# Kernel tuning notes

Measured on AMD Instinct MI355X. Metric: run time of the kernel, lower is better.

The kernel has to match this reference:

```python
import jax, jax.numpy as jnp
import numpy as np

N_HEADS = 16
MAX_SEQ_LEN = 2048


def _rotary_tables(d_k, max_seq_len):
    # Rotary.__init__: dim//4 frequencies followed by dim//4 zeros -> dim//2 entries
    freqs = (1.0 / 10000.0) ** jnp.linspace(0.0, 1.0, d_k // 4, dtype=jnp.float32)
    freqs = jnp.concatenate([freqs, jnp.zeros(d_k // 4, dtype=jnp.float32)])
    theta = jnp.arange(max_seq_len, dtype=jnp.float32)[:, None] * freqs[None, :]  # [S, d_k//2]
    return jnp.cos(theta), jnp.sin(theta)


def _apply_rotary_bug_faithful(u, cos, sin):
    # u: [B, H, T, Dk]. Original Rotary indexes cos/sin by u.size(-3) == n_heads,
    # so the rotation angle depends on the HEAD index and broadcasts over time.
    H = u.shape[1]
    c = cos[None, :H, None, :]  # [1, H, 1, Dk//2]
    s = sin[None, :H, None, :]
    u1, u2 = jnp.split(u.astype(jnp.float32), 2, axis=-1)
    y1 = u1 * c + u2 * s
    y2 = -u1 * s + u2 * c
    return jnp.concatenate([y1, y2], axis=-1).astype(u.dtype)


def setup_inputs() -> dict:
    key = jax.random.key(0)
    k1, k2, k3 = jax.random.split(key, 3)
    d_model = 2048
    B, T = 2, 2048
    x = jax.random.normal(k1, (B, T, d_model), dtype=jnp.float32)
    w_qkv = jax.random.normal(k2, (3 * d_model, d_model), dtype=jnp.float32) * (1.0 / np.sqrt(d_model))
    w_o = jax.random.normal(k3, (d_model, d_model), dtype=jnp.float32) * (1.0 / np.sqrt(d_model))
    return {"x": x, "w_qkv": w_qkv, "w_o": w_o}


def reference(x, w_qkv, w_o):
    B, T, D = x.shape
    H = N_HEADS
    dk = D // H
    cos, sin = _rotary_tables(dk, MAX_SEQ_LEN)

    # Fused QKV projection (Linear, no bias): [B,T,3D]
    qkv = jnp.einsum('btd,ed->bte', x, w_qkv)
    qkv = qkv.reshape(B, T, 3, H, dk).transpose(2, 0, 3, 1, 4)  # [3,B,H,T,dk]
    Q, K, V = qkv[0], qkv[1], qkv[2]

    Q = _apply_rotary_bug_faithful(Q, cos, sin)
    K = _apply_rotary_bug_faithful(K, cos, sin)

    # Causal scaled dot-product attention (eval mode -> dropout_p = 0)
    scale = 1.0 / np.sqrt(dk)
    scores = jnp.einsum('bhqd,bhkd->bhqk', Q, K) * scale
    causal = jnp.tril(jnp.ones((T, T), dtype=bool))
    scores = jnp.where(causal[None, None], scores, jnp.finfo(scores.dtype).min)
    attn = jax.nn.softmax(scores, axis=-1)
    out = jnp.einsum('bhqk,bhkd->bhqd', attn, V)  # [B,H,T,dk]
    out = out.transpose(0, 2, 1, 3).reshape(B, T, D)
    return jnp.einsum('btd,ed->bte', out, w_o)
```

## Files before the change

kernel.cpp:

```cpp
#include <hip/hip_runtime.h>

typedef unsigned short u16;
typedef short bf16x8 __attribute__((ext_vector_type(8)));
typedef float f32x4 __attribute__((ext_vector_type(4)));
typedef unsigned short u16x4 __attribute__((ext_vector_type(4)));

#define QK_SCALE 0.08838834764831845f

__device__ __forceinline__ u16 f2bf(float f) {
  unsigned u = __float_as_uint(f);
  u += 0x7fffu + ((u >> 16) & 1u);
  return (u16)(u >> 16);
}
__device__ __forceinline__ float bf2f(u16 h) { return __uint_as_float(((unsigned)h) << 16); }

__device__ __forceinline__ void gld_lds16(const u16* g, u16* l) {
  __builtin_amdgcn_global_load_lds(
      (const __attribute__((address_space(1))) void*)g,
      (__attribute__((address_space(3))) void*)l, 16, 0, 0);
}

__global__ void cvt_bf16_kernel(const float* __restrict__ in, u16* __restrict__ out, int n4) {
  int i = blockIdx.x * 256 + threadIdx.x;
  if (i >= n4) return;
  const float4 v = reinterpret_cast<const float4*>(in)[i];
  u16x4 o;
  o[0] = f2bf(v.x); o[1] = f2bf(v.y); o[2] = f2bf(v.z); o[3] = f2bf(v.w);
  reinterpret_cast<u16x4*>(out)[i] = o;
}

template<int MODE>
__global__ __launch_bounds__(256) void gemm_bt_kernel(
    const u16* __restrict__ A, const u16* __restrict__ Bw, int Kdim, int n_out,
    u16* __restrict__ q_out, u16* __restrict__ k_out, u16* __restrict__ v_out,
    float* __restrict__ f_out)
{
  __shared__ __align__(16) u16 As[128 * 32];
  __shared__ __align__(16) u16 Bs[128 * 32];
  const int t = threadIdx.x;
  const int lane = t & 63;
  const int w = t >> 6;
  const int wr = w >> 1, wc = w & 1;
  const int m0 = blockIdx.x * 128, n0 = blockIdx.y * 128;

  f32x4 acc[4][4];
#pragma unroll
  for (int m = 0; m < 4; ++m)
#pragma unroll
    for (int n = 0; n < 4; ++n)
#pragma unroll
      for (int i = 0; i < 4; ++i) acc[m][n][i] = 0.0f;

  const int ob0 = w * 1024 + lane * 16;
  const int row0 = ob0 >> 6;
  const int cole0 = (ob0 & 63) >> 1;
  const u16* gA0 = A + (size_t)(m0 + row0) * Kdim + cole0;
  const u16* gA1 = gA0 + (size_t)64 * Kdim;
  const u16* gB0 = Bw + (size_t)(n0 + row0) * Kdim + cole0;
  const u16* gB1 = gB0 + (size_t)64 * Kdim;
  u16* lA = As + w * 512;
  u16* lB = Bs + w * 512;

  const int l15 = lane & 15;
  const int kb = (lane >> 4) * 8;

  for (int k0 = 0; k0 < Kdim; k0 += 32) {
    __syncthreads();
    gld_lds16(gA0, lA);
    gld_lds16(gA1, lA + 2048);
    gld_lds16(gB0, lB);
    gld_lds16(gB1, lB + 2048);
    gA0 += 32; gA1 += 32; gB0 += 32; gB1 += 32;
    __syncthreads();
    bf16x8 a[4], b[4];
#pragma unroll
    for (int m = 0; m < 4; ++m)
      a[m] = *reinterpret_cast<const bf16x8*>(As + (wr * 64 + m * 16 + l15) * 32 + kb);
#pragma unroll
    for (int n = 0; n < 4; ++n)
      b[n] = *reinterpret_cast<const bf16x8*>(Bs + (wc * 64 + n * 16 + l15) * 32 + kb);
#pragma unroll
    for (int m = 0; m < 4; ++m)
#pragma unroll
      for (int n = 0; n < 4; ++n)
        acc[m][n] = __builtin_amdgcn_mfma_f32_16x16x32_bf16(a[m], b[n], acc[m][n], 0, 0, 0);
  }

  const int rb = wr * 64 + ((lane >> 4) << 2);
  const int cbs = wc * 64 + l15;
  if (MODE == 0) {
#pragma unroll
    for (int n = 0; n < 4; ++n) {
      const int e = n0 + cbs + n * 16;
      const int which = e >> 11;
      const int h = (e >> 7) & 15;
      const int d = e & 127;
      u16* dst = (which == 0) ? q_out : (which == 1) ? k_out : v_out;
#pragma unroll
      for (int m = 0; m < 4; ++m)
#pragma unroll
        for (int r = 0; r < 4; ++r) {
          const int bt = m0 + rb + m * 16 + r;
          const int bb = bt >> 11, tt = bt & 2047;
          dst[((size_t)(bb * 16 + h) * 2048 + tt) * 128 + d] = f2bf(acc[m][n][r]);
        }
    }
  } else {
#pragma unroll
    for (int m = 0; m < 4; ++m)
#pragma unroll
      for (int r = 0; r < 4; ++r) {
        const int row = m0 + rb + m * 16 + r;
#pragma unroll
        for (int n = 0; n < 4; ++n)
          f_out[(size_t)row * n_out + n0 + cbs + n * 16] = acc[m][n][r];
      }
  }
}

__global__ void rotary_kernel(u16* __restrict__ Qb, u16* __restrict__ Kb) {
  const int idx = blockIdx.x * 256 + threadIdx.x;
  const int j4 = idx & 15;
  const int row = idx >> 4;
  const int h = (row >> 11) & 15;
  const size_t base = (size_t)row * 128 + j4 * 4;
  float c[4], s[4];
#pragma unroll
  for (int i = 0; i < 4; ++i) {
    const int j = j4 * 4 + i;
    const float fr = (j < 32) ? __expf(-0.2971077539f * (float)j) : 0.0f;
    const float th = (float)h * fr;
    c[i] = cosf(th); s[i] = sinf(th);
  }
  {
    u16x4 u1 = *reinterpret_cast<u16x4*>(Qb + base);
    u16x4 u2 = *reinterpret_cast<u16x4*>(Qb + base + 64);
    u16x4 y1, y2;
#pragma unroll
    for (int i = 0; i < 4; ++i) {
      const float a = bf2f(u1[i]), b = bf2f(u2[i]);
      y1[i] = f2bf((a * c[i] + b * s[i]) * QK_SCALE);
      y2[i] = f2bf((b * c[i] - a * s[i]) * QK_SCALE);
    }
    *reinterpret_cast<u16x4*>(Qb + base) = y1;
    *reinterpret_cast<u16x4*>(Qb + base + 64) = y2;
  }
  {
    u16x4 u1 = *reinterpret_cast<u16x4*>(Kb + base);
    u16x4 u2 = *reinterpret_cast<u16x4*>(Kb + base + 64);
    u16x4 y1, y2;
#pragma unroll
    for (int i = 0; i < 4; ++i) {
      const float a = bf2f(u1[i]), b = bf2f(u2[i]);
      y1[i] = f2bf(a * c[i] + b * s[i]);
      y2[i] = f2bf(b * c[i] - a * s[i]);
    }
    *reinterpret_cast<u16x4*>(Kb + base) = y1;
    *reinterpret_cast<u16x4*>(Kb + base + 64) = y2;
  }
}

__global__ void transpose_v_kernel(const u16* __restrict__ V, u16* __restrict__ Vt) {
  __shared__ u16 tile[64][65];
  const int d0 = blockIdx.x * 64;
  const int t0 = blockIdx.y * 64;
  const int bh = blockIdx.z;
  const u16* src = V + (size_t)bh * (2048 * 128);
  u16* dst = Vt + (size_t)bh * (128 * 2048);
  const int tid = threadIdx.x;
  const int c4 = (tid & 15) * 4;
  const int r0 = tid >> 4;
#pragma unroll
  for (int p = 0; p < 4; ++p) {
    const int row = r0 + p * 16;
    const u16x4 v = *reinterpret_cast<const u16x4*>(src + (size_t)(t0 + row) * 128 + d0 + c4);
    tile[row][c4] = v[0]; tile[row][c4 + 1] = v[1];
    tile[row][c4 + 2] = v[2]; tile[row][c4 + 3] = v[3];
  }
  __syncthreads();
#pragma unroll
  for (int p = 0; p < 4; ++p) {
    const int dr = r0 + p * 16;
    u16x4 ov;
    ov[0] = tile[c4][dr]; ov[1] = tile[c4 + 1][dr];
    ov[2] = tile[c4 + 2][dr]; ov[3] = tile[c4 + 3][dr];
    *reinterpret_cast<u16x4*>(dst + (size_t)(d0 + dr) * 2048 + t0 + c4) = ov;
  }
}

__global__ __launch_bounds__(256) void attn_kernel(
    const u16* __restrict__ Q, const u16* __restrict__ K,
    const u16* __restrict__ Vt, u16* __restrict__ O)
{
  __shared__ __align__(16) u16 k_lds[2][64 * 128];
  __shared__ __align__(16) u16 v_lds[2][128 * 64];
  __shared__ __align__(16) u16 p_lds[4][1024];
  const int t = threadIdx.x, lane = t & 63, w = t >> 6;
  const int bh = blockIdx.y;
  const int bx = blockIdx.x;
  const int l15 = lane & 15, lhi = lane >> 4;
  const size_t qkb = (size_t)bh * (2048 * 128);
  const u16* Kg = K + qkb;
  const u16* Vg = Vt + (size_t)bh * (size_t)(128 * 2048);
  char* pw = (char*)(&p_lds[w][0]);
  const int bb = bh >> 4, h = bh & 15;
  const int kxor = (l15 & 7) << 4;

  auto stage = [&](int buf, int k0) {
#pragma unroll
    for (int ii = 0; ii < 4; ++ii) {
      const int i = w * 4 + ii;
      const int krow = i * 4 + lhi;
      gld_lds16(Kg + (size_t)(k0 + krow) * 128 + (size_t)((l15 ^ (krow & 7)) * 8),
                &k_lds[buf][i * 512]);
    }
#pragma unroll
    for (int ii = 0; ii < 4; ++ii) {
      const int i = w * 4 + ii;
      const int vrow = i * 8 + (lane >> 3);
      gld_lds16(Vg + (size_t)vrow * 2048 + k0 + (size_t)(((lane & 7) ^ (vrow & 7)) * 8),
                &v_lds[buf][i * 512]);
    }
  };

  for (int half = 0; half < 2; ++half) {
    const int qt = half ? (31 - bx) : bx;
    const int q0 = qt * 64 + w * 16;
    bf16x8 aq[4];
    {
      const u16* qp = Q + qkb + (size_t)(q0 + l15) * 128 + lhi * 8;
#pragma unroll
      for (int ks = 0; ks < 4; ++ks) aq[ks] = *reinterpret_cast<const bf16x8*>(qp + ks * 32);
    }
    f32x4 o[8];
#pragma unroll
    for (int dt = 0; dt < 8; ++dt)
#pragma unroll
      for (int i = 0; i < 4; ++i) o[dt][i] = 0.0f;
    float mrow[4] = {-1e30f, -1e30f, -1e30f, -1e30f};
    float lrow[4] = {0.f, 0.f, 0.f, 0.f};
    const int rbase = q0 + (lhi << 2);
    const int ktmax = qt;

    __syncthreads();
    stage(0, 0);
    int cur = 0;
    for (int kt = 0; kt <= ktmax; ++kt) {
      __syncthreads();
      if (kt < ktmax) stage(cur ^ 1, (kt + 1) * 64);

      const char* kbb = (const char*)(&k_lds[cur][0]);
      f32x4 s4[4];
#pragma unroll
      for (int nt = 0; nt < 4; ++nt)
#pragma unroll
        for (int i = 0; i < 4; ++i) s4[nt][i] = 0.0f;
#pragma unroll
      for (int nt = 0; nt < 4; ++nt) {
        const int krow = nt * 16 + l15;
#pragma unroll
        for (int ks = 0; ks < 4; ++ks) {
          const bf16x8 bk = *reinterpret_cast<const bf16x8*>(
              kbb + krow * 256 + ((ks * 64 + lhi * 16) ^ kxor));
          s4[nt] = __builtin_amdgcn_mfma_f32_16x16x32_bf16(aq[ks], bk, s4[nt], 0, 0, 0);
        }
      }
      if (kt == ktmax) {
#pragma unroll
        for (int nt = 0; nt < 4; ++nt) {
          const int col = kt * 64 + nt * 16 + l15;
#pragma unroll
          for (int r = 0; r < 4; ++r)
            if (col > rbase + r) s4[nt][r] = -1e30f;
        }
      }
      float alpha[4];
#pragma unroll
      for (int r = 0; r < 4; ++r) {
        float mx = fmaxf(fmaxf(s4[0][r], s4[1][r]), fmaxf(s4[2][r], s4[3][r]));
        mx = fmaxf(mx, __shfl_xor(mx, 1));
        mx = fmaxf(mx, __shfl_xor(mx, 2));
        mx = fmaxf(mx, __shfl_xor(mx, 4));
        mx = fmaxf(mx, __shfl_xor(mx, 8));
        const float mn = fmaxf(mrow[r], mx);
        alpha[r] = __expf(mrow[r] - mn);
        mrow[r] = mn;
      }
      float ps[4] = {0.f, 0.f, 0.f, 0.f};
#pragma unroll
      for (int nt = 0; nt < 4; ++nt)
#pragma unroll
        for (int r = 0; r < 4; ++r) {
          const float p = __expf(s4[nt][r] - mrow[r]);
          ps[r] += p;
          const int prow = (lhi << 2) + r;
          const int cbyte = (nt * 16 + l15) * 2;
          *(u16*)(pw + prow * 128 + (cbyte ^ ((prow & 7) << 4))) = f2bf(p);
        }
#pragma unroll
      for (int r = 0; r < 4; ++r) {
        float rs = ps[r];
        rs += __shfl_xor(rs, 1);
        rs += __shfl_xor(rs, 2);
        rs += __shfl_xor(rs, 4);
        rs += __shfl_xor(rs, 8);
        lrow[r] = lrow[r] * alpha[r] + rs;
#pragma unroll
        for (int dt = 0; dt < 8; ++dt) o[dt][r] *= alpha[r];
      }
      const char* vbb = (const char*)(&v_lds[cur][0]);
#pragma unroll
      for (int ks2 = 0; ks2 < 2; ++ks2) {
        const bf16x8 ap = *reinterpret_cast<const bf16x8*>(
            pw + l15 * 128 + ((ks2 * 64 + (lhi << 4)) ^ kxor));
#pragma unroll
        for (int dt = 0; dt < 8; ++dt) {
          const int vrow = dt * 16 + l15;
          const bf16x8 bv = *reinterpret_cast<const bf16x8*>(
              vbb + vrow * 128 + ((ks2 * 64 + lhi * 16) ^ kxor));
          o[dt] = __builtin_amdgcn_mfma_f32_16x16x32_bf16(ap, bv, o[dt], 0, 0, 0);
        }
      }
      cur ^= 1;
    }
#pragma unroll
    for (int r = 0; r < 4; ++r) {
      const float inv = 1.0f / lrow[r];
      const int row = rbase + r;
      u16* op = O + (size_t)(bb * 2048 + row) * 2048 + h * 128 + l15;
#pragma unroll
      for (int dt = 0; dt < 8; ++dt) op[dt * 16] = f2bf(o[dt][r] * inv);
    }
  }
}

extern "C" void kernel_launch(void* const* d_in, const int* in_sizes, int n_in,
                              void* d_out, int out_size, void* d_ws, size_t ws_size,
                              hipStream_t stream) {
  const float* x = (const float*)d_in[0];
  const float* wqkv = (const float*)d_in[1];
  const float* wo = (const float*)d_in[2];
  float* out = (float*)d_out;
  u16* ws = (u16*)d_ws;

  u16* xb = ws;
  u16* wqkvb = xb + 8388608;
  u16* wob = wqkvb + 12582912;
  u16* Qb = wob + 4194304;
  u16* Kb = Qb + 8388608;
  u16* Vb = Kb + 8388608;
  u16* Vtb = wqkvb;
  u16* attn = xb;

  cvt_bf16_kernel<<<8192, 256, 0, stream>>>(x, xb, 2097152);
  cvt_bf16_kernel<<<12288, 256, 0, stream>>>(wqkv, wqkvb, 3145728);
  cvt_bf16_kernel<<<4096, 256, 0, stream>>>(wo, wob, 1048576);

  gemm_bt_kernel<0><<<dim3(32, 48), 256, 0, stream>>>(xb, wqkvb, 2048, 0, Qb, Kb, Vb, nullptr);

  rotary_kernel<<<4096, 256, 0, stream>>>(Qb, Kb);
  transpose_v_kernel<<<dim3(2, 32, 32), 256, 0, stream>>>(Vb, Vtb);

  attn_kernel<<<dim3(16, 32), 256, 0, stream>>>(Qb, Kb, Vtb, attn);

  gemm_bt_kernel<1><<<dim3(32, 16), 256, 0, stream>>>(attn, wob, 2048, 2048, nullptr, nullptr, nullptr, out);
}
```

Measured before the change: 327.2 us.

## Add 256x256 double-buffered 8-wave GEMM for the QKV projection

Replaces the QKV projection GEMM with a new kernel. It uses 256x256 output tiles, 512 threads (8 waves), K tiles of 64, double-buffered LDS with an XOR-swizzled layout, and async global-to-LDS loads that overlap the MFMA work in phases. The loop raises wave priority around the MFMA phases with s_setprio and uses explicit barriers and vmcnt waits. The goal is more data reuse per tile and hiding global load latency, in exchange for 128KB of LDS per block and more register pressure. The output projection keeps the old simple GEMM, now without the unused mode template.

After: 323.3 us. About the same (-1.2%).

```diff
diff --git a/kernel.cpp b/kernel.cpp
--- a/kernel.cpp
+++ b/kernel.cpp
@@ -30,13 +30,167 @@
 }
 
 template<int MODE>
-__global__ __launch_bounds__(256) void gemm_bt_kernel(
+__global__ __launch_bounds__(512, 2) void gemm8p_kernel(
     const u16* __restrict__ A, const u16* __restrict__ Bw, int Kdim, int n_out,
     u16* __restrict__ q_out, u16* __restrict__ k_out, u16* __restrict__ v_out,
     float* __restrict__ f_out)
 {
-  __shared__ __align__(16) u16 As[128 * 32];
-  __shared__ __align__(16) u16 Bs[128 * 32];
+  __shared__ __align__(16) u16 As[2][256 * 64];
+  __shared__ __align__(16) u16 Bs[2][256 * 64];
+  const int t = threadIdx.x, lane = t & 63, w = t >> 6;
+  const int wr = w >> 2, wc = w & 3;
+  const int l15 = lane & 15, lhi = lane >> 4;
+  const int m0 = blockIdx.x * 256, n0 = blockIdx.y * 256;
+  const int NT = Kdim >> 6;
+
+  const int srow = w * 8 + (lane >> 3);
+  const int gchunk = (lane & 7) ^ (srow & 7);
+  const size_t gcol = (size_t)gchunk * 8;
+
+  auto stageA2 = [&](int buf, int kt2, int half) {
+    const size_t kb = (size_t)kt2 * 64 + gcol;
+#pragma unroll
+    for (int i = 0; i < 2; ++i) {
+      const int ro = half * 128 + i * 64;
+      gld_lds16(A + (size_t)(m0 + srow + ro) * Kdim + kb, &As[buf][(w * 8 + ro) * 64]);
+    }
+  };
+  auto stageB4 = [&](int buf, int kt2) {
+    const size_t kb = (size_t)kt2 * 64 + gcol;
+#pragma unroll
+    for (int ro = 0; ro < 256; ro += 64)
+      gld_lds16(Bw + (size_t)(n0 + srow + ro) * Kdim + kb, &Bs[buf][(w * 8 + ro) * 64]);
+  };
+
+  const int arow0 = (wr * 128 + l15) * 64;
+  const int brow0 = (wc * 64 + l15) * 64;
+  const int koff0 = ((0 + lhi) ^ (l15 & 7)) * 8;
+  const int koff1 = ((4 + lhi) ^ (l15 & 7)) * 8;
+
+  f32x4 acc[8][4];
+#pragma unroll
+  for (int m = 0; m < 8; ++m)
+#pragma unroll
+    for (int n = 0; n < 4; ++n)
+#pragma unroll
+      for (int i = 0; i < 4; ++i) acc[m][n][i] = 0.0f;
+
+  stageA2(0, 0, 0); stageA2(0, 0, 1);
+  stageB4(0, 0);
+  if (NT > 1) { stageA2(1, 1, 0); stageA2(1, 1, 1); }
+  asm volatile("s_waitcnt vmcnt(4)" ::: "memory");
+  __builtin_amdgcn_s_barrier();
+
+  for (int kt = 0; kt < NT; ++kt) {
+    const int cur = kt & 1;
+    const u16* __restrict__ Ac = &As[cur][0];
+    const u16* __restrict__ Bc = &Bs[cur][0];
+    bf16x8 aK1[4], a2K1[4], b0[4], b1[4];
+    {
+      bf16x8 aK0[4];
+#pragma unroll
+      for (int m = 0; m < 4; ++m) {
+        aK0[m] = *reinterpret_cast<const bf16x8*>(Ac + arow0 + m * 1024 + koff0);
+        aK1[m] = *reinterpret_cast<const bf16x8*>(Ac + arow0 + m * 1024 + koff1);
+      }
+#pragma unroll
+      for (int n = 0; n < 4; ++n)
+        b0[n] = *reinterpret_cast<const bf16x8*>(Bc + brow0 + n * 1024 + koff0);
+      if (kt + 1 < NT) stageB4(cur ^ 1, kt + 1);
+      __builtin_amdgcn_s_barrier();
+      asm volatile("s_waitcnt lgkmcnt(0)" ::: "memory");
+      __builtin_amdgcn_s_setprio(1);
+#pragma unroll
+      for (int m = 0; m < 4; ++m)
+#pragma unroll
+        for (int n = 0; n < 4; ++n)
+          acc[m][n] = __builtin_amdgcn_mfma_f32_16x16x32_bf16(aK0[m], b0[n], acc[m][n], 0, 0, 0);
+      __builtin_amdgcn_s_setprio(0);
+      __builtin_amdgcn_s_barrier();
+    }
+    {
+      bf16x8 a2K0[4];
+#pragma unroll
+      for (int m = 0; m < 4; ++m) {
+        a2K0[m] = *reinterpret_cast<const bf16x8*>(Ac + arow0 + (m + 4) * 1024 + koff0);
+        a2K1[m] = *reinterpret_cast<const bf16x8*>(Ac + arow0 + (m + 4) * 1024 + koff1);
+      }
+#pragma unroll
+      for (int n = 0; n < 4; ++n)
+        b1[n] = *reinterpret_cast<const bf16x8*>(Bc + brow0 + n * 1024 + koff1);
+      __builtin_amdgcn_s_barrier();
+      asm volatile("s_waitcnt lgkmcnt(0)" ::: "memory");
+      __builtin_amdgcn_s_setprio(1);
+#pragma unroll
+      for (int m = 0; m < 4; ++m)
+#pragma unroll
+        for (int n = 0; n < 4; ++n)
+          acc[m + 4][n] = __builtin_amdgcn_mfma_f32_16x16x32_bf16(a2K0[m], b0[n], acc[m + 4][n], 0, 0, 0);
+      __builtin_amdgcn_s_setprio(0);
+      __builtin_amdgcn_s_barrier();
+    }
+    if (kt + 2 < NT) stageA2(cur, kt + 2, 0);
+    __builtin_amdgcn_s_barrier();
+    __builtin_amdgcn_s_setprio(1);
+#pragma unroll
+    for (int m = 0; m < 4; ++m)
+#pragma unroll
+      for (int n = 0; n < 4; ++n)
+        acc[m][n] = __builtin_amdgcn_mfma_f32_16x16x32_bf16(aK1[m], b1[n], acc[m][n], 0, 0, 0);
+    __builtin_amdgcn_s_setprio(0);
+    __builtin_amdgcn_s_barrier();
+    if (kt + 2 < NT) stageA2(cur, kt + 2, 1);
+    __builtin_amdgcn_s_barrier();
+    __builtin_amdgcn_s_setprio(1);
+#pragma unroll
+    for (int m = 0; m < 4; ++m)
+#pragma unroll
+      for (int n = 0; n < 4; ++n)
+        acc[m + 4][n] = __builtin_amdgcn_mfma_f32_16x16x32_bf16(a2K1[m], b1[n], acc[m + 4][n], 0, 0, 0);
+    __builtin_amdgcn_s_setprio(0);
+    if (kt < NT - 2) { asm volatile("s_waitcnt vmcnt(4)" ::: "memory"); }
+    else             { asm volatile("s_waitcnt vmcnt(0)" ::: "memory"); }
+    __builtin_amdgcn_s_barrier();
+  }
+
+  const int rb = wr * 128 + lhi * 4;
+  const int cb = wc * 64 + l15;
+  if (MODE == 0) {
+#pragma unroll
+    for (int n = 0; n < 4; ++n) {
+      const int e = n0 + cb + n * 16;
+      const int which = e >> 11;
+      const int h = (e >> 7) & 15;
+      const int d = e & 127;
+      u16* dst = (which == 0) ? q_out : (which == 1) ? k_out : v_out;
+#pragma unroll
+      for (int m = 0; m < 8; ++m)
+#pragma unroll
+        for (int r = 0; r < 4; ++r) {
+          const int bt = m0 + rb + m * 16 + r;
+          const int bb = bt >> 11, tt = bt & 2047;
+          dst[((size_t)(bb * 16 + h) * 2048 + tt) * 128 + d] = f2bf(acc[m][n][r]);
+        }
+    }
+  } else {
+#pragma unroll
+    for (int m = 0; m < 8; ++m)
+#pragma unroll
+      for (int r = 0; r < 4; ++r) {
+        const int row = m0 + rb + m * 16 + r;
+#pragma unroll
+        for (int n = 0; n < 4; ++n)
+          f_out[(size_t)row * n_out + n0 + cb + n * 16] = acc[m][n][r];
+      }
+  }
+}
+
+__global__ __launch_bounds__(256) void gemm_bt_kernel(
+    const u16* __restrict__ A, const u16* __restrict__ Bw, int Kdim, int n_out,
+    float* __restrict__ f_out)
+{
+  __shared__ __align__(16) u16 Asl[128 * 32];
+  __shared__ __align__(16) u16 Bsl[128 * 32];
   const int t = threadIdx.x;
   const int lane = t & 63;
   const int w = t >> 6;
@@ -58,8 +212,8 @@
   const u16* gA1 = gA0 + (size_t)64 * Kdim;
   const u16* gB0 = Bw + (size_t)(n0 + row0) * Kdim + cole0;
   const u16* gB1 = gB0 + (size_t)64 * Kdim;
-  u16* lA = As + w * 512;
-  u16* lB = Bs + w * 512;
+  u16* lA = Asl + w * 512;
+  u16* lB = Bsl + w * 512;
 
   const int l15 = lane & 15;
   const int kb = (lane >> 4) * 8;
@@ -75,10 +229,10 @@
     bf16x8 a[4], b[4];
 #pragma unroll
     for (int m = 0; m < 4; ++m)
-      a[m] = *reinterpret_cast<const bf16x8*>(As + (wr * 64 + m * 16 + l15) * 32 + kb);
+      a[m] = *reinterpret_cast<const bf16x8*>(Asl + (wr * 64 + m * 16 + l15) * 32 + kb);
 #pragma unroll
     for (int n = 0; n < 4; ++n)
-      b[n] = *reinterpret_cast<const bf16x8*>(Bs + (wc * 64 + n * 16 + l15) * 32 + kb);
+      b[n] = *reinterpret_cast<const bf16x8*>(Bsl + (wc * 64 + n * 16 + l15) * 32 + kb);
 #pragma unroll
     for (int m = 0; m < 4; ++m)
 #pragma unroll
@@ -88,34 +242,15 @@
 
   const int rb = wr * 64 + ((lane >> 4) << 2);
   const int cbs = wc * 64 + l15;
-  if (MODE == 0) {
-#pragma unroll
-    for (int n = 0; n < 4; ++n) {
-      const int e = n0 + cbs + n * 16;
-      const int which = e >> 11;
-      const int h = (e >> 7) & 15;
-      const int d = e & 127;
-      u16* dst = (which == 0) ? q_out : (which == 1) ? k_out : v_out;
-#pragma unroll
-      for (int m = 0; m < 4; ++m)
-#pragma unroll
-        for (int r = 0; r < 4; ++r) {
-          const int bt = m0 + rb + m * 16 + r;
-          const int bb = bt >> 11, tt = bt & 2047;
-          dst[((size_t)(bb * 16 + h) * 2048 + tt) * 128 + d] = f2bf(acc[m][n][r]);
-        }
-    }
-  } else {
-#pragma unroll
-    for (int m = 0; m < 4; ++m)
-#pragma unroll
-      for (int r = 0; r < 4; ++r) {
-        const int row = m0 + rb + m * 16 + r;
-#pragma unroll
-        for (int n = 0; n < 4; ++n)
-          f_out[(size_t)row * n_out + n0 + cbs + n * 16] = acc[m][n][r];
-      }
-  }
+#pragma unroll
+  for (int m = 0; m < 4; ++m)
+#pragma unroll
+    for (int r = 0; r < 4; ++r) {
+      const int row = m0 + rb + m * 16 + r;
+#pragma unroll
+      for (int n = 0; n < 4; ++n)
+        f_out[(size_t)row * n_out + n0 + cbs + n * 16] = acc[m][n][r];
+    }
 }
 
 __global__ void rotary_kernel(u16* __restrict__ Qb, u16* __restrict__ Kb) {
@@ -356,12 +491,12 @@
   cvt_bf16_kernel<<<12288, 256, 0, stream>>>(wqkv, wqkvb, 3145728);
   cvt_bf16_kernel<<<4096, 256, 0, stream>>>(wo, wob, 1048576);
 
-  gemm_bt_kernel<0><<<dim3(32, 48), 256, 0, stream>>>(xb, wqkvb, 2048, 0, Qb, Kb, Vb, nullptr);
+  gemm8p_kernel<0><<<dim3(16, 24), 512, 0, stream>>>(xb, wqkvb, 2048, 0, Qb, Kb, Vb, nullptr);
 
   rotary_kernel<<<4096, 256, 0, stream>>>(Qb, Kb);
   transpose_v_kernel<<<dim3(2, 32, 32), 256, 0, stream>>>(Vb, Vtb);
 
   attn_kernel<<<dim3(16, 32), 256, 0, stream>>>(Qb, Kb, Vtb, attn);
 
-  gemm_bt_kernel<1><<<dim3(32, 16), 256, 0, stream>>>(attn, wob, 2048, 2048, nullptr, nullptr, nullptr, out);
-}
+  gemm_bt_kernel<<<dim3(32, 16), 256, 0, stream>>>(attn, wob, 2048, 2048, out);
+}
```

## Fold rotary into QKV weights and use a 256x256 pipelined GEMM for QKV

Applied to the files above, without the earlier changes.

The rotary rotation and the Q scale depend only on the head index, so they are applied to the rows of w_qkv during the bf16 conversion. This removes the separate rotary pass over Q and K. The QKV projection now runs on a new 512-thread GEMM with 256x256 tiles, double-buffered LDS, XOR swizzle and barrier-interleaved MFMA phases. Its output is row-major [B*T, 6144], which attention and the V transpose read with strided addressing, so the head-scatter epilogue goes away. The trade-off is higher register and LDS pressure and slightly different rounding, because the rotation is applied before bf16 quantization rather than after.

After: 451.5 us. 38.0% more time.

```diff
diff --git a/kernel.cpp b/kernel.cpp
--- a/kernel.cpp
+++ b/kernel.cpp
@@ -29,14 +29,155 @@
   reinterpret_cast<u16x4*>(out)[i] = o;
 }
 
+__global__ void rotw_kernel(const float* __restrict__ w, u16* __restrict__ wb) {
+  const int i = blockIdx.x * 256 + threadIdx.x;
+  const int k4 = i & 511;
+  const int j = (i >> 9) & 63;
+  const int h = (i >> 15) & 15;
+  const int which = i >> 19;
+  const size_t e1 = (size_t)which * 2048 + h * 128 + j;
+  const size_t e2 = e1 + 64;
+  const float fr = (j < 32) ? __expf(-0.2971077539f * (float)j) : 0.0f;
+  float s, c;
+  __sincosf((float)h * fr, &s, &c);
+  const float scale = (which == 0) ? QK_SCALE : 1.0f;
+  const float4 a = reinterpret_cast<const float4*>(w + e1 * 2048)[k4];
+  const float4 b = reinterpret_cast<const float4*>(w + e2 * 2048)[k4];
+  u16x4 o1, o2;
+  o1[0] = f2bf((a.x * c + b.x * s) * scale);
+  o1[1] = f2bf((a.y * c + b.y * s) * scale);
+  o1[2] = f2bf((a.z * c + b.z * s) * scale);
+  o1[3] = f2bf((a.w * c + b.w * s) * scale);
+  o2[0] = f2bf((b.x * c - a.x * s) * scale);
+  o2[1] = f2bf((b.y * c - a.y * s) * scale);
+  o2[2] = f2bf((b.z * c - a.z * s) * scale);
+  o2[3] = f2bf((b.w * c - a.w * s) * scale);
+  reinterpret_cast<u16x4*>(wb + e1 * 2048)[k4] = o1;
+  reinterpret_cast<u16x4*>(wb + e2 * 2048)[k4] = o2;
+}
+
 template<int MODE>
+__global__ __launch_bounds__(512, 2) void gemm8p_kernel(
+    const u16* __restrict__ A, const u16* __restrict__ Bw, int Kdim, int n_out,
+    u16* __restrict__ c_bf16, float* __restrict__ c_f32)
+{
+  __shared__ __align__(16) u16 As[2][256 * 64];
+  __shared__ __align__(16) u16 Bs[2][256 * 64];
+  const int t = threadIdx.x, lane = t & 63, w = t >> 6;
+  const int wr = w >> 2, wc = w & 3;
+  const int l15 = lane & 15, lhi = lane >> 4;
+  const int m0 = blockIdx.x * 256, n0 = blockIdx.y * 256;
+  const int NT = Kdim >> 6, NI = NT >> 1;
+
+  const int srow = w * 8 + (lane >> 3);
+  const size_t gcol = (size_t)(((lane & 7) ^ (srow & 7)) * 8);
+
+#define STA(buf, kt, h) { \
+    const size_t kb_ = (size_t)(kt) * 64 + gcol; \
+    gld_lds16(A + (size_t)(m0 + srow + (h) * 128) * Kdim + kb_, &As[buf][(w * 8 + (h) * 128) * 64]); \
+    gld_lds16(A + (size_t)(m0 + srow + (h) * 128 + 64) * Kdim + kb_, &As[buf][(w * 8 + (h) * 128 + 64) * 64]); }
+#define STB(buf, kt, h) { \
+    const size_t kb_ = (size_t)(kt) * 64 + gcol; \
+    gld_lds16(Bw + (size_t)(n0 + srow + (h) * 128) * Kdim + kb_, &Bs[buf][(w * 8 + (h) * 128) * 64]); \
+    gld_lds16(Bw + (size_t)(n0 + srow + (h) * 128 + 64) * Kdim + kb_, &Bs[buf][(w * 8 + (h) * 128 + 64) * 64]); }
+
+  const int arow = (wr * 128 + l15) * 64;
+  const int brow = (wc * 64 + l15) * 64;
+  const int ko0 = (lhi ^ (l15 & 7)) * 8;
+  const int ko1 = ((4 + lhi) ^ (l15 & 7)) * 8;
+
+#define RDA(buf, mq, ko, dst) { _Pragma("unroll") \
+    for (int m_ = 0; m_ < 4; ++m_) dst[m_] = *reinterpret_cast<const bf16x8*>(&As[buf][arow + ((mq) + m_) * 1024 + (ko)]); }
+#define RDB(buf, ko, dst) { _Pragma("unroll") \
+    for (int n_ = 0; n_ < 4; ++n_) dst[n_] = *reinterpret_cast<const bf16x8*>(&Bs[buf][brow + n_ * 1024 + (ko)]); }
+#define MMA(a_, b_, mq) { __builtin_amdgcn_s_setprio(1); _Pragma("unroll") \
+    for (int m_ = 0; m_ < 4; ++m_) { _Pragma("unroll") for (int n_ = 0; n_ < 4; ++n_) \
+      acc[(mq) + m_][n_] = __builtin_amdgcn_mfma_f32_16x16x32_bf16(a_[m_], b_[n_], acc[(mq) + m_][n_], 0, 0, 0); } \
+    __builtin_amdgcn_s_setprio(0); }
+#define BAR() __builtin_amdgcn_s_barrier()
+#define LGK0() asm volatile("s_waitcnt lgkmcnt(0)" ::: "memory")
+
+  f32x4 acc[8][4];
+#pragma unroll
+  for (int m = 0; m < 8; ++m)
+#pragma unroll
+    for (int n = 0; n < 4; ++n)
+#pragma unroll
+      for (int i = 0; i < 4; ++i) acc[m][n][i] = 0.0f;
+
+  bf16x8 aq[4], aqn[4], b0[4], b1[4];
+
+  STB(0, 0, 0); STA(0, 0, 0); STA(0, 0, 1); STB(0, 0, 1);
+  STB(1, 1, 0); STA(1, 1, 0);
+  asm volatile("s_waitcnt vmcnt(4)" ::: "memory");
+  BAR();
+  RDA(0, 0, ko0, aq); RDB(0, ko0, b0);
+
+  for (int i = 0; i < NI; ++i) {
+    const int t1 = 2 * i + 1;
+    const bool g = (i + 1 < NI);
+    STA(1, t1, 1);
+    RDA(0, 4, ko0, aqn);
+    BAR(); LGK0(); MMA(aq, b0, 0); BAR();
+    STB(1, t1, 1);
+    RDA(0, 0, ko1, aq); RDB(0, ko1, b1);
+    BAR(); LGK0(); MMA(aqn, b0, 4); BAR();
+    if (g) { STB(0, t1 + 1, 0); }
+    RDA(0, 4, ko1, aqn);
+    if (g) { asm volatile("s_waitcnt vmcnt(2)" ::: "memory"); }
+    else   { asm volatile("s_waitcnt vmcnt(0)" ::: "memory"); }
+    BAR(); LGK0(); MMA(aq, b1, 0); BAR();
+    if (g) { STA(0, t1 + 1, 0); }
+    RDA(1, 0, ko0, aq); RDB(1, ko0, b0);
+    BAR(); LGK0(); MMA(aqn, b1, 4); BAR();
+    if (g) { STA(0, t1 + 1, 1); }
+    RDA(1, 4, ko0, aqn);
+    BAR(); LGK0(); MMA(aq, b0, 0); BAR();
+    if (g) { STB(0, t1 + 1, 1); }
+    RDA(1, 0, ko1, aq); RDB(1, ko1, b1);
+    BAR(); LGK0(); MMA(aqn, b0, 4); BAR();
+    if (g) { STB(1, t1 + 2, 0); }
+    RDA(1, 4, ko1, aqn);
+    if (g) { asm volatile("s_waitcnt vmcnt(2)" ::: "memory"); }
+    else   { asm volatile("s_waitcnt vmcnt(0)" ::: "memory"); }
+    BAR(); LGK0(); MMA(aq, b1, 0); BAR();
+    if (g) { STA(1, t1 + 2, 0); }
+    if (g) { RDA(0, 0, ko0, aq); RDB(0, ko0, b0); }
+    BAR(); LGK0(); MMA(aqn, b1, 4); BAR();
+  }
+
+  const int rb = wr * 128 + lhi * 4;
+  const int cb = wc * 64 + l15;
+#pragma unroll
+  for (int m = 0; m < 8; ++m)
+#pragma unroll
+    for (int r = 0; r < 4; ++r) {
+      const size_t row = (size_t)(m0 + rb + m * 16 + r);
+      if (MODE == 0) {
+#pragma unroll
+        for (int n = 0; n < 4; ++n)
+          c_bf16[row * n_out + n0 + cb + n * 16] = f2bf(acc[m][n][r]);
+      } else {
+#pragma unroll
+        for (int n = 0; n < 4; ++n)
+          c_f32[row * n_out + n0 + cb + n * 16] = acc[m][n][r];
+      }
+    }
+#undef STA
+#undef STB
+#undef RDA
+#undef RDB
+#undef MMA
+#undef BAR
+#undef LGK0
+}
+
 __global__ __launch_bounds__(256) void gemm_bt_kernel(
     const u16* __restrict__ A, const u16* __restrict__ Bw, int Kdim, int n_out,
-    u16* __restrict__ q_out, u16* __restrict__ k_out, u16* __restrict__ v_out,
     float* __restrict__ f_out)
 {
-  __shared__ __align__(16) u16 As[128 * 32];
-  __shared__ __align__(16) u16 Bs[128 * 32];
+  __shared__ __align__(16) u16 Asl[128 * 32];
+  __shared__ __align__(16) u16 Bsl[128 * 32];
   const int t = threadIdx.x;
   const int lane = t & 63;
   const int w = t >> 6;
@@ -58,8 +199,8 @@
   const u16* gA1 = gA0 + (size_t)64 * Kdim;
   const u16* gB0 = Bw + (size_t)(n0 + row0) * Kdim + cole0;
   const u16* gB1 = gB0 + (size_t)64 * Kdim;
-  u16* lA = As + w * 512;
-  u16* lB = Bs + w * 512;
+  u16* lA = Asl + w * 512;
+  u16* lB = Bsl + w * 512;
 
   const int l15 = lane & 15;
   const int kb = (lane >> 4) * 8;
@@ -75,10 +216,10 @@
     bf16x8 a[4], b[4];
 #pragma unroll
     for (int m = 0; m < 4; ++m)
-      a[m] = *reinterpret_cast<const bf16x8*>(As + (wr * 64 + m * 16 + l15) * 32 + kb);
+      a[m] = *reinterpret_cast<const bf16x8*>(Asl + (wr * 64 + m * 16 + l15) * 32 + kb);
 #pragma unroll
     for (int n = 0; n < 4; ++n)
-      b[n] = *reinterpret_cast<const bf16x8*>(Bs + (wc * 64 + n * 16 + l15) * 32 + kb);
+      b[n] = *reinterpret_cast<const bf16x8*>(Bsl + (wc * 64 + n * 16 + l15) * 32 + kb);
 #pragma unroll
     for (int m = 0; m < 4; ++m)
 #pragma unroll
@@ -88,84 +229,24 @@
 
   const int rb = wr * 64 + ((lane >> 4) << 2);
   const int cbs = wc * 64 + l15;
-  if (MODE == 0) {
-#pragma unroll
-    for (int n = 0; n < 4; ++n) {
-      const int e = n0 + cbs + n * 16;
-      const int which = e >> 11;
-      const int h = (e >> 7) & 15;
-      const int d = e & 127;
-      u16* dst = (which == 0) ? q_out : (which == 1) ? k_out : v_out;
-#pragma unroll
-      for (int m = 0; m < 4; ++m)
-#pragma unroll
-        for (int r = 0; r < 4; ++r) {
-          const int bt = m0 + rb + m * 16 + r;
-          const int bb = bt >> 11, tt = bt & 2047;
-          dst[((size_t)(bb * 16 + h) * 2048 + tt) * 128 + d] = f2bf(acc[m][n][r]);
-        }
-    }
-  } else {
-#pragma unroll
-    for (int m = 0; m < 4; ++m)
-#pragma unroll
-      for (int r = 0; r < 4; ++r) {
-        const int row = m0 + rb + m * 16 + r;
-#pragma unroll
-        for (int n = 0; n < 4; ++n)
-          f_out[(size_t)row * n_out + n0 + cbs + n * 16] = acc[m][n][r];
-      }
-  }
-}
-
-__global__ void rotary_kernel(u16* __restrict__ Qb, u16* __restrict__ Kb) {
-  const int idx = blockIdx.x * 256 + threadIdx.x;
-  const int j4 = idx & 15;
-  const int row = idx >> 4;
-  const int h = (row >> 11) & 15;
-  const size_t base = (size_t)row * 128 + j4 * 4;
-  float c[4], s[4];
-#pragma unroll
-  for (int i = 0; i < 4; ++i) {
-    const int j = j4 * 4 + i;
-    const float fr = (j < 32) ? __expf(-0.2971077539f * (float)j) : 0.0f;
-    const float th = (float)h * fr;
-    c[i] = cosf(th); s[i] = sinf(th);
-  }
-  {
-    u16x4 u1 = *reinterpret_cast<u16x4*>(Qb + base);
-    u16x4 u2 = *reinterpret_cast<u16x4*>(Qb + base + 64);
-    u16x4 y1, y2;
-#pragma unroll
-    for (int i = 0; i < 4; ++i) {
-      const float a = bf2f(u1[i]), b = bf2f(u2[i]);
-      y1[i] = f2bf((a * c[i] + b * s[i]) * QK_SCALE);
-      y2[i] = f2bf((b * c[i] - a * s[i]) * QK_SCALE);
-    }
-    *reinterpret_cast<u16x4*>(Qb + base) = y1;
-    *reinterpret_cast<u16x4*>(Qb + base + 64) = y2;
-  }
-  {
-    u16x4 u1 = *reinterpret_cast<u16x4*>(Kb + base);
-    u16x4 u2 = *reinterpret_cast<u16x4*>(Kb + base + 64);
-    u16x4 y1, y2;
-#pragma unroll
-    for (int i = 0; i < 4; ++i) {
-      const float a = bf2f(u1[i]), b = bf2f(u2[i]);
-      y1[i] = f2bf(a * c[i] + b * s[i]);
-      y2[i] = f2bf(b * c[i] - a * s[i]);
-    }
-    *reinterpret_cast<u16x4*>(Kb + base) = y1;
-    *reinterpret_cast<u16x4*>(Kb + base + 64) = y2;
-  }
-}
-
-__global__ void transpose_v_kernel(const u16* __restrict__ V, u16* __restrict__ Vt) {
+#pragma unroll
+  for (int m = 0; m < 4; ++m)
+#pragma unroll
+    for (int r = 0; r < 4; ++r) {
+      const int row = m0 + rb + m * 16 + r;
+#pragma unroll
+      for (int n = 0; n < 4; ++n)
+        f_out[(size_t)row * n_out + n0 + cbs + n * 16] = acc[m][n][r];
+    }
+}
+
+__global__ void transpose_v_kernel(const u16* __restrict__ QKV, u16* __restrict__ Vt) {
   __shared__ u16 tile[64][65];
   const int d0 = blockIdx.x * 64;
   const int t0 = blockIdx.y * 64;
   const int bh = blockIdx.z;
-  const u16* src = V + (size_t)bh * (2048 * 128);
+  const int bb = bh >> 4, h = bh & 15;
+  const u16* src = QKV + (size_t)(bb * 2048) * 6144 + 4096 + h * 128;
   u16* dst = Vt + (size_t)bh * (128 * 2048);
   const int tid = threadIdx.x;
   const int c4 = (tid & 15) * 4;
@@ -173,7 +254,7 @@
 #pragma unroll
   for (int p = 0; p < 4; ++p) {
     const int row = r0 + p * 16;
-    const u16x4 v = *reinterpret_cast<const u16x4*>(src + (size_t)(t0 + row) * 128 + d0 + c4);
+    const u16x4 v = *reinterpret_cast<const u16x4*>(src + (size_t)(t0 + row) * 6144 + d0 + c4);
     tile[row][c4] = v[0]; tile[row][c4 + 1] = v[1];
     tile[row][c4 + 2] = v[2]; tile[row][c4 + 3] = v[3];
   }
@@ -189,8 +270,7 @@
 }
 
 __global__ __launch_bounds__(256) void attn_kernel(
-    const u16* __restrict__ Q, const u16* __restrict__ K,
-    const u16* __restrict__ Vt, u16* __restrict__ O)
+    const u16* __restrict__ QKV, const u16* __restrict__ Vt, u16* __restrict__ O)
 {
   __shared__ __align__(16) u16 k_lds[2][64 * 128];
   __shared__ __align__(16) u16 v_lds[2][128 * 64];
@@ -199,11 +279,11 @@
   const int bh = blockIdx.y;
   const int bx = blockIdx.x;
   const int l15 = lane & 15, lhi = lane >> 4;
-  const size_t qkb = (size_t)bh * (2048 * 128);
-  const u16* Kg = K + qkb;
+  const int bb = bh >> 4, h = bh & 15;
+  const u16* Qg = QKV + (size_t)(bb * 2048) * 6144 + h * 128;
+  const u16* Kg = QKV + (size_t)(bb * 2048) * 6144 + 2048 + h * 128;
   const u16* Vg = Vt + (size_t)bh * (size_t)(128 * 2048);
   char* pw = (char*)(&p_lds[w][0]);
-  const int bb = bh >> 4, h = bh & 15;
   const int kxor = (l15 & 7) << 4;
 
   auto stage = [&](int buf, int k0) {
@@ -211,7 +291,7 @@
     for (int ii = 0; ii < 4; ++ii) {
       const int i = w * 4 + ii;
       const int krow = i * 4 + lhi;
-      gld_lds16(Kg + (size_t)(k0 + krow) * 128 + (size_t)((l15 ^ (krow & 7)) * 8),
+      gld_lds16(Kg + (size_t)(k0 + krow) * 6144 + (size_t)((l15 ^ (krow & 7)) * 8),
                 &k_lds[buf][i * 512]);
     }
 #pragma unroll
@@ -228,7 +308,7 @@
     const int q0 = qt * 64 + w * 16;
     bf16x8 aq[4];
     {
-      const u16* qp = Q + qkb + (size_t)(q0 + l15) * 128 + lhi * 8;
+      const u16* qp = Qg + (size_t)(q0 + l15) * 6144 + lhi * 8;
 #pragma unroll
       for (int ks = 0; ks < 4; ++ks) aq[ks] = *reinterpret_cast<const bf16x8*>(qp + ks * 32);
     }
@@ -346,22 +426,21 @@
   u16* xb = ws;
   u16* wqkvb = xb + 8388608;
   u16* wob = wqkvb + 12582912;
-  u16* Qb = wob + 4194304;
-  u16* Kb = Qb + 8388608;
-  u16* Vb = Kb + 8388608;
+  u16* qkvb = wob + 4194304;
   u16* Vtb = wqkvb;
   u16* attn = xb;
 
   cvt_bf16_kernel<<<8192, 256, 0, stream>>>(x, xb, 2097152);
-  cvt_bf16_kernel<<<12288, 256, 0, stream>>>(wqkv, wqkvb, 3145728);
+  rotw_kernel<<<4096, 256, 0, stream>>>(wqkv, wqkvb);
+  cvt_bf16_kernel<<<4096, 256, 0, stream>>>(wqkv + (size_t)4096 * 2048,
+                                            wqkvb + (size_t)4096 * 2048, 1048576);
   cvt_bf16_kernel<<<4096, 256, 0, stream>>>(wo, wob, 1048576);
 
-  gemm_bt_kernel<0><<<dim3(32, 48), 256, 0, stream>>>(xb, wqkvb, 2048, 0, Qb, Kb, Vb, nullptr);
-
-  rotary_kernel<<<4096, 256, 0, stream>>>(Qb, Kb);
-  transpose_v_kernel<<<dim3(2, 32, 32), 256, 0, stream>>>(Vb, Vtb);
-
-  attn_kernel<<<dim3(16, 32), 256, 0, stream>>>(Qb, Kb, Vtb, attn);
-
-  gemm_bt_kernel<1><<<dim3(32, 16), 256, 0, stream>>>(attn, wob, 2048, 2048, nullptr, nullptr, nullptr, out);
-}
+  gemm8p_kernel<0><<<dim3(16, 24), 512, 0, stream>>>(xb, wqkvb, 2048, 6144, qkvb, nullptr);
+
+  transpose_v_kernel<<<dim3(2, 32, 32), 256, 0, stream>>>(qkvb, Vtb);
+
+  attn_kernel<<<dim3(16, 32), 256, 0, stream>>>(qkvb, Vtb, attn);
+
+  gemm_bt_kernel<<<dim3(32, 16), 256, 0, stream>>>(attn, wob, 2048, 2048, out);
+}
```
